# Kernel optimization log

Measured on AMD Instinct MI355X. Metric: run time of the kernel, lower is better.

Reference implementation:

```python
import jax, jax.numpy as jnp
import numpy as np

N = 100000   # nodes
E = 1600000  # edges (before self loops)
IN, HID, OUT = 128, 128, 64


def setup_inputs() -> dict:
    key = jax.random.key(0)
    ks = jax.random.split(key, 5)
    x = jax.random.normal(ks[0], (N, IN), dtype=jnp.float32)
    edge_index = jax.random.randint(ks[1], (2, E), 0, N, dtype=jnp.int32)
    W1 = jax.random.normal(ks[2], (IN, HID), dtype=jnp.float32) * (1.0 / np.sqrt(IN))
    b1 = jnp.zeros((HID,), dtype=jnp.float32)
    W2 = jax.random.normal(ks[3], (HID, OUT), dtype=jnp.float32) * (1.0 / np.sqrt(HID))
    b2 = jnp.zeros((OUT,), dtype=jnp.float32)
    return {"x": x, "edge_index": edge_index, "W1": W1, "b1": b1, "W2": W2, "b2": b2}


def _gcn_conv(x, W, b, src, dst, norm):
    # linear transform first (small GEMM), then normalized scatter-add aggregation
    h = x @ W                                   # [N, d_out]
    msg = h[src] * norm[:, None]                # [E+N, d_out] gathered messages
    agg = jax.ops.segment_sum(msg, dst, num_segments=N)
    return agg + b


def reference(x, edge_index, W1, b1, W2, b2):
    loops = jnp.arange(N, dtype=edge_index.dtype)
    src = jnp.concatenate([edge_index[0], loops])   # add self loops (PyG GCNConv default)
    dst = jnp.concatenate([edge_index[1], loops])
    # symmetric normalization D^{-1/2} (A+I) D^{-1/2}
    deg = jax.ops.segment_sum(jnp.ones_like(dst, dtype=x.dtype), dst, num_segments=N)
    dinv = jnp.where(deg > 0, jax.lax.rsqrt(deg), 0.0)
    norm = dinv[src] * dinv[dst]                # [E+N]

    h = _gcn_conv(x, W1, b1, src, dst, norm)
    h = jax.nn.relu(h)
    out = _gcn_conv(h, W2, b2, src, dst, norm)
    return out
```

## Files before the change

### kernel.cpp

```cpp
#include <hip/hip_runtime.h>
#include <hip/hip_bf16.h>

#define IN_DIM  128
#define HID_DIM 128
#define OUT_DIM 64

typedef unsigned short ushort_t;
struct ushort4_t { ushort_t x, y, z, w; };
typedef __attribute__((ext_vector_type(8))) short bf16x8;
typedef __attribute__((ext_vector_type(4))) float f32x4;

__device__ __forceinline__ float bf2f(ushort_t u) {
    return __uint_as_float(((unsigned int)u) << 16);
}
__device__ __forceinline__ short f2bf_s(float v) {
    __hip_bfloat16 t = __float2bfloat16(v);
    return *(short*)&t;
}
__device__ __forceinline__ unsigned int pack2(float a, float b) {
    return ((unsigned int)(ushort_t)f2bf_s(b) << 16) | (ushort_t)f2bf_s(a);
}

__global__ __launch_bounds__(256, 2) void fused_gemm1_count(
        const float* __restrict__ x, const float* __restrict__ W,
        unsigned int* __restrict__ h,
        const int* __restrict__ dst, int* __restrict__ cnt, int* __restrict__ rank,
        int N, int E, int NT) {
    const int bid = blockIdx.x;
    const int tid = threadIdx.x;

    if (bid & 1) {
        const int lane = tid & 63;
        const int m    = lane & 15;
        const int quad = lane >> 4;
        const int gw   = (bid >> 1) * 4 + (tid >> 6);
        const int NW   = 1024;

        bf16x8 a[8][4];
        #pragma unroll
        for (int ct = 0; ct < 8; ++ct)
            #pragma unroll
            for (int kc = 0; kc < 4; ++kc)
                #pragma unroll
                for (int j = 0; j < 8; ++j)
                    a[ct][kc][j] = f2bf_s(W[(size_t)(kc * 32 + quad * 8 + j) * HID_DIM + ct * 16 + m]);

        for (int t = gw; t < NT; t += NW) {
            const int n0 = t * 16;
            int node = n0 + m; if (node >= N) node = N - 1;
            const float* xr = x + (size_t)node * IN_DIM + quad * 8;
            f32x4 acc[8];
            #pragma unroll
            for (int ct = 0; ct < 8; ++ct) acc[ct] = (f32x4){0.f, 0.f, 0.f, 0.f};
            #pragma unroll
            for (int kc = 0; kc < 4; ++kc) {
                const float4 v0 = *(const float4*)(xr + kc * 32);
                const float4 v1 = *(const float4*)(xr + kc * 32 + 4);
                bf16x8 b;
                b[0] = f2bf_s(v0.x); b[1] = f2bf_s(v0.y); b[2] = f2bf_s(v0.z); b[3] = f2bf_s(v0.w);
                b[4] = f2bf_s(v1.x); b[5] = f2bf_s(v1.y); b[6] = f2bf_s(v1.z); b[7] = f2bf_s(v1.w);
                #pragma unroll
                for (int ct = 0; ct < 8; ++ct)
                    acc[ct] = __builtin_amdgcn_mfma_f32_16x16x32_bf16(a[ct][kc], b, acc[ct], 0, 0, 0);
            }
            if (n0 + m < N) {
                unsigned int* o = h + (size_t)(n0 + m) * (HID_DIM / 2) + quad * 2;
                #pragma unroll
                for (int ct = 0; ct < 8; ++ct) {
                    uint2 pv;
                    pv.x = pack2(acc[ct][0], acc[ct][1]);
                    pv.y = pack2(acc[ct][2], acc[ct][3]);
                    *(uint2*)(o + ct * 8) = pv;
                }
            }
        }
    } else {
        const int ct = (bid >> 1) * 256 + tid;
        const int CT = 256 * 256;
        const int nq = E >> 2;
        const int4* d4 = (const int4*)dst;
        for (int q = ct; q < nq; q += CT) {
            const int4 d = d4[q];
            int4 r;
            r.x = atomicAdd(&cnt[d.x], 1);
            r.y = atomicAdd(&cnt[d.y], 1);
            r.z = atomicAdd(&cnt[d.z], 1);
            r.w = atomicAdd(&cnt[d.w], 1);
            ((int4*)rank)[q] = r;
        }
        for (int e = (nq << 2) + ct; e < E; e += CT)
            rank[e] = atomicAdd(&cnt[dst[e]], 1);
    }
}

__global__ void scan_partial(const int* __restrict__ cnt, int* __restrict__ bsum,
                             float* __restrict__ dinv, int N) {
    __shared__ int wsum[4];
    const int t = threadIdx.x;
    const int base = blockIdx.x * 2048 + t * 8;
    int s = 0;
    #pragma unroll
    for (int i = 0; i < 8; ++i) {
        if (base + i < N) {
            const int c = cnt[base + i];
            dinv[base + i] = rsqrtf((float)(c + 1));
            s += (c + 3) & ~3;
        }
    }
    #pragma unroll
    for (int off = 32; off > 0; off >>= 1) s += __shfl_down(s, off);
    const int lane = t & 63, w = t >> 6;
    if (lane == 0) wsum[w] = s;
    __syncthreads();
    if (t == 0) bsum[blockIdx.x] = wsum[0] + wsum[1] + wsum[2] + wsum[3];
}

__global__ void scan_write(const int* __restrict__ cnt, const int* __restrict__ bsum,
                           int* __restrict__ row_start, int2* __restrict__ pack, int N) {
    __shared__ int wsum[4];
    __shared__ int blockoff;
    const int t = threadIdx.x;
    if (t < 64) {
        int a = 0;
        for (int idx = t; idx < blockIdx.x; idx += 64) a += bsum[idx];
        #pragma unroll
        for (int off = 32; off > 0; off >>= 1) a += __shfl_down(a, off);
        if (t == 0) blockoff = a;
    }
    const int base = blockIdx.x * 2048 + t * 8;
    int c[8], v[8];
    #pragma unroll
    for (int i = 0; i < 8; ++i) {
        c[i] = (base + i < N) ? cnt[base + i] : 0;
        v[i] = (c[i] + 3) & ~3;
    }
    int s = v[0] + v[1] + v[2] + v[3] + v[4] + v[5] + v[6] + v[7];
    const int lane = t & 63, w = t >> 6;
    int incl = s;
    #pragma unroll
    for (int off = 1; off < 64; off <<= 1) {
        int u = __shfl_up(incl, off);
        if (lane >= off) incl += u;
    }
    if (lane == 63) wsum[w] = incl;
    __syncthreads();
    int woff = 0;
    for (int i = 0; i < w; ++i) woff += wsum[i];
    int run = blockoff + woff + (incl - s);
    const int2 zr = {0, 0};
    #pragma unroll
    for (int i = 0; i < 8; ++i) {
        if (base + i < N) {
            row_start[base + i] = run;
            for (int p = c[i]; p < v[i]; ++p) pack[run + p] = zr;
            run += v[i];
        }
    }
}

__global__ void fill_pack4(const int* __restrict__ src, const int* __restrict__ dst,
                           const int* __restrict__ rank, const int* __restrict__ row_start,
                           const float* __restrict__ dinv, int E, int2* __restrict__ pack) {
    const int q = blockIdx.x * blockDim.x + threadIdx.x;
    const int nq = E >> 2;
    if (q < nq) {
        const int4 s = ((const int4*)src)[q];
        const int4 d = ((const int4*)dst)[q];
        const int4 r = ((const int4*)rank)[q];
        int2 p;
        p.x = s.x; p.y = __float_as_int(dinv[s.x] * dinv[d.x]);
        pack[row_start[d.x] + r.x] = p;
        p.x = s.y; p.y = __float_as_int(dinv[s.y] * dinv[d.y]);
        pack[row_start[d.y] + r.y] = p;
        p.x = s.z; p.y = __float_as_int(dinv[s.z] * dinv[d.z]);
        pack[row_start[d.z] + r.z] = p;
        p.x = s.w; p.y = __float_as_int(dinv[s.w] * dinv[d.w]);
        pack[row_start[d.w] + r.w] = p;
    }
    if (q == 0) {
        for (int e = nq << 2; e < E; ++e) {
            int2 p;
            p.x = src[e]; p.y = __float_as_int(dinv[src[e]] * dinv[dst[e]]);
            pack[row_start[dst[e]] + rank[e]] = p;
        }
    }
}

__global__ __launch_bounds__(256) void gemm2_mfma(
        const ushort_t* __restrict__ agg,
        const float* __restrict__ W2, unsigned int* __restrict__ h2,
        int N, int NT, int NW) {
    const int tid  = threadIdx.x;
    const int lane = tid & 63;
    const int m    = lane & 15;
    const int quad = lane >> 4;
    const int gw   = blockIdx.x * 4 + (tid >> 6);

    bf16x8 a[4][4];
    #pragma unroll
    for (int ct = 0; ct < 4; ++ct)
        #pragma unroll
        for (int kc = 0; kc < 4; ++kc)
            #pragma unroll
            for (int j = 0; j < 8; ++j)
                a[ct][kc][j] = f2bf_s(W2[(size_t)(kc * 32 + quad * 8 + j) * OUT_DIM + ct * 16 + m]);

    for (int t = gw; t < NT; t += NW) {
        const int n0 = t * 16;
        int node = n0 + m; if (node >= N) node = N - 1;
        const ushort_t* ar = agg + (size_t)node * HID_DIM + quad * 8;
        f32x4 acc[4];
        #pragma unroll
        for (int ct = 0; ct < 4; ++ct) acc[ct] = (f32x4){0.f, 0.f, 0.f, 0.f};
        #pragma unroll
        for (int kc = 0; kc < 4; ++kc) {
            const bf16x8 b = *(const bf16x8*)(ar + kc * 32);
            #pragma unroll
            for (int ct = 0; ct < 4; ++ct)
                acc[ct] = __builtin_amdgcn_mfma_f32_16x16x32_bf16(a[ct][kc], b, acc[ct], 0, 0, 0);
        }
        if (n0 + m < N) {
            unsigned int* o = h2 + (size_t)(n0 + m) * (OUT_DIM / 2) + quad * 2;
            #pragma unroll
            for (int ct = 0; ct < 4; ++ct) {
                uint2 pv;
                pv.x = pack2(acc[ct][0], acc[ct][1]);
                pv.y = pack2(acc[ct][2], acc[ct][3]);
                *(uint2*)(o + ct * 8) = pv;
            }
        }
    }
}

template<int D, bool BF16_OUT, bool RELU>
__global__ void gather_bf16(const ushort_t* __restrict__ h, const int2* __restrict__ pack,
                            const int* __restrict__ row_start, const int* __restrict__ cnt,
                            const float* __restrict__ dinv, const float* __restrict__ bias,
                            int N, void* __restrict__ outv) {
    const int TPN = D / 4;
    const int NPB = 256 / TPN;
    const int t = threadIdx.x;
    const int node = blockIdx.x * NPB + t / TPN;
    if (node >= N) return;
    const int f = (t & (TPN - 1)) * 4;
    const float dd = dinv[node];

    const ushort4_t self = *(const ushort4_t*)(h + (size_t)node * D + f);
    const float sn = dd * dd;
    float4 acc;
    acc.x = bf2f(self.x) * sn; acc.y = bf2f(self.y) * sn;
    acc.z = bf2f(self.z) * sn; acc.w = bf2f(self.w) * sn;
    const float4 bv = *(const float4*)(bias + f);
    acc.x += bv.x; acc.y += bv.y; acc.z += bv.z; acc.w += bv.w;

    const int2* pk = pack + row_start[node];
    const int cpad = (cnt[node] + 3) & ~3;
    for (int e = 0; e < cpad; e += 4) {
        const int4 a = *(const int4*)(pk + e);
        const int4 b = *(const int4*)(pk + e + 2);
        {
            const ushort4_t v = *(const ushort4_t*)(h + (size_t)a.x * D + f);
            const float n = __int_as_float(a.y);
            acc.x += bf2f(v.x) * n; acc.y += bf2f(v.y) * n;
            acc.z += bf2f(v.z) * n; acc.w += bf2f(v.w) * n;
        }
        {
            const ushort4_t v = *(const ushort4_t*)(h + (size_t)a.z * D + f);
            const float n = __int_as_float(a.w);
            acc.x += bf2f(v.x) * n; acc.y += bf2f(v.y) * n;
            acc.z += bf2f(v.z) * n; acc.w += bf2f(v.w) * n;
        }
        {
            const ushort4_t v = *(const ushort4_t*)(h + (size_t)b.x * D + f);
            const float n = __int_as_float(b.y);
            acc.x += bf2f(v.x) * n; acc.y += bf2f(v.y) * n;
            acc.z += bf2f(v.z) * n; acc.w += bf2f(v.w) * n;
        }
        {
            const ushort4_t v = *(const ushort4_t*)(h + (size_t)b.z * D + f);
            const float n = __int_as_float(b.w);
            acc.x += bf2f(v.x) * n; acc.y += bf2f(v.y) * n;
            acc.z += bf2f(v.z) * n; acc.w += bf2f(v.w) * n;
        }
    }
    if (RELU) {
        acc.x = fmaxf(acc.x, 0.f); acc.y = fmaxf(acc.y, 0.f);
        acc.z = fmaxf(acc.z, 0.f); acc.w = fmaxf(acc.w, 0.f);
    }
    if (BF16_OUT) {
        unsigned int* out = (unsigned int*)outv;
        uint2 pv;
        pv.x = pack2(acc.x, acc.y);
        pv.y = pack2(acc.z, acc.w);
        *(uint2*)(out + ((size_t)node * D + f) / 2) = pv;
    } else {
        float* out = (float*)outv;
        *(float4*)(out + (size_t)node * D + f) = acc;
    }
}

extern "C" void kernel_launch(void* const* d_in, const int* in_sizes, int n_in,
                              void* d_out, int out_size, void* d_ws, size_t ws_size,
                              hipStream_t stream) {
    const float* x   = (const float*)d_in[0];
    const int*   ei  = (const int*)  d_in[1];
    const float* W1  = (const float*)d_in[2];
    const float* b1  = (const float*)d_in[3];
    const float* W2  = (const float*)d_in[4];
    const float* b2  = (const float*)d_in[5];
    float* out = (float*)d_out;

    const int N = in_sizes[0] / IN_DIM;
    const int E = in_sizes[1] / 2;
    const int* src = ei;
    const int* dst = ei + E;

    const int PACK_CAP = E + 4 * N;
    float* dinv      = (float*)d_ws;
    int*   cnt       = (int*)(dinv + N);
    int*   row_start = cnt + N;
    int*   bsum      = row_start + N;
    size_t off       = (size_t)(3 * N + 1024);
    off = (off + 3) & ~(size_t)3;
    int2*  pack      = (int2*)((int*)d_ws + off);
    unsigned int* h1 = (unsigned int*)(pack + PACK_CAP);
    unsigned int* agg1 = h1 + (size_t)N * (HID_DIM / 2);
    int*   rank      = (int*)agg1;
    unsigned int* h2 = h1;

    const int B = 256;
    const int S = (N + 2047) / 2048;
    const int NT = (N + 15) / 16;

    hipMemsetAsync(cnt, 0, (size_t)N * sizeof(int), stream);
    fused_gemm1_count<<<512, 256, 0, stream>>>(x, W1, h1, dst, cnt, rank, N, E, NT);

    scan_partial<<<S, 256, 0, stream>>>(cnt, bsum, dinv, N);
    scan_write<<<S, 256, 0, stream>>>(cnt, bsum, row_start, pack, N);

    fill_pack4<<<((E >> 2) + B - 1) / B, B, 0, stream>>>(src, dst, rank, row_start, dinv, E, pack);

    gather_bf16<HID_DIM, true, true><<<(N + 7) / 8, 256, 0, stream>>>(
        (const ushort_t*)h1, pack, row_start, cnt, dinv, b1, N, (void*)agg1);

    gemm2_mfma<<<768, 256, 0, stream>>>(
        (const ushort_t*)agg1, W2, h2, N, NT, 768 * 4);

    gather_bf16<OUT_DIM, false, false><<<(N + 15) / 16, 256, 0, stream>>>(
        (const ushort_t*)h2, pack, row_start, cnt, dinv, b2, N, (void*)out);
}
```

Baseline: 312.2 us.

## Replace atomic CSR build with two-level bucket sort by destination

```diff
diff --git a/kernel.cpp b/kernel.cpp
--- a/kernel.cpp
+++ b/kernel.cpp
@@ -4,6 +4,8 @@
 #define IN_DIM  128
 #define HID_DIM 128
 #define OUT_DIM 64
+#define NBUK 1024
+#define NB1  256
 
 typedef unsigned short ushort_t;
 struct ushort4_t { ushort_t x, y, z, w; };
@@ -21,121 +23,160 @@
     return ((unsigned int)(ushort_t)f2bf_s(b) << 16) | (ushort_t)f2bf_s(a);
 }
 
-__global__ __launch_bounds__(256, 2) void fused_gemm1_count(
+__global__ __launch_bounds__(256, 2) void gemm1_mfma(
         const float* __restrict__ x, const float* __restrict__ W,
-        unsigned int* __restrict__ h,
-        const int* __restrict__ dst, int* __restrict__ cnt, int* __restrict__ rank,
-        int N, int E, int NT) {
-    const int bid = blockIdx.x;
-    const int tid = threadIdx.x;
-
-    if (bid & 1) {
-        const int lane = tid & 63;
-        const int m    = lane & 15;
-        const int quad = lane >> 4;
-        const int gw   = (bid >> 1) * 4 + (tid >> 6);
-        const int NW   = 1024;
-
-        bf16x8 a[8][4];
-        #pragma unroll
-        for (int ct = 0; ct < 8; ++ct)
-            #pragma unroll
-            for (int kc = 0; kc < 4; ++kc)
-                #pragma unroll
-                for (int j = 0; j < 8; ++j)
-                    a[ct][kc][j] = f2bf_s(W[(size_t)(kc * 32 + quad * 8 + j) * HID_DIM + ct * 16 + m]);
-
-        for (int t = gw; t < NT; t += NW) {
-            const int n0 = t * 16;
-            int node = n0 + m; if (node >= N) node = N - 1;
-            const float* xr = x + (size_t)node * IN_DIM + quad * 8;
-            f32x4 acc[8];
-            #pragma unroll
-            for (int ct = 0; ct < 8; ++ct) acc[ct] = (f32x4){0.f, 0.f, 0.f, 0.f};
-            #pragma unroll
-            for (int kc = 0; kc < 4; ++kc) {
-                const float4 v0 = *(const float4*)(xr + kc * 32);
-                const float4 v1 = *(const float4*)(xr + kc * 32 + 4);
-                bf16x8 b;
-                b[0] = f2bf_s(v0.x); b[1] = f2bf_s(v0.y); b[2] = f2bf_s(v0.z); b[3] = f2bf_s(v0.w);
-                b[4] = f2bf_s(v1.x); b[5] = f2bf_s(v1.y); b[6] = f2bf_s(v1.z); b[7] = f2bf_s(v1.w);
-                #pragma unroll
-                for (int ct = 0; ct < 8; ++ct)
-                    acc[ct] = __builtin_amdgcn_mfma_f32_16x16x32_bf16(a[ct][kc], b, acc[ct], 0, 0, 0);
+        unsigned int* __restrict__ h, int N, int NT, int NW) {
+    const int tid  = threadIdx.x;
+    const int lane = tid & 63;
+    const int m    = lane & 15;
+    const int quad = lane >> 4;
+    const int gw   = blockIdx.x * 4 + (tid >> 6);
+
+    bf16x8 a[8][4];
+    #pragma unroll
+    for (int ct = 0; ct < 8; ++ct)
+        #pragma unroll
+        for (int kc = 0; kc < 4; ++kc)
+            #pragma unroll
+            for (int j = 0; j < 8; ++j)
+                a[ct][kc][j] = f2bf_s(W[(size_t)(kc * 32 + quad * 8 + j) * HID_DIM + ct * 16 + m]);
+
+    for (int t = gw; t < NT; t += NW) {
+        const int n0 = t * 16;
+        int node = n0 + m; if (node >= N) node = N - 1;
+        const float* xr = x + (size_t)node * IN_DIM + quad * 8;
+        f32x4 acc[8];
+        #pragma unroll
+        for (int ct = 0; ct < 8; ++ct) acc[ct] = (f32x4){0.f, 0.f, 0.f, 0.f};
+        #pragma unroll
+        for (int kc = 0; kc < 4; ++kc) {
+            const float4 v0 = *(const float4*)(xr + kc * 32);
+            const float4 v1 = *(const float4*)(xr + kc * 32 + 4);
+            bf16x8 b;
+            b[0] = f2bf_s(v0.x); b[1] = f2bf_s(v0.y); b[2] = f2bf_s(v0.z); b[3] = f2bf_s(v0.w);
+            b[4] = f2bf_s(v1.x); b[5] = f2bf_s(v1.y); b[6] = f2bf_s(v1.z); b[7] = f2bf_s(v1.w);
+            #pragma unroll
+            for (int ct = 0; ct < 8; ++ct)
+                acc[ct] = __builtin_amdgcn_mfma_f32_16x16x32_bf16(a[ct][kc], b, acc[ct], 0, 0, 0);
+        }
+        if (n0 + m < N) {
+            unsigned int* o = h + (size_t)(n0 + m) * (HID_DIM / 2) + quad * 2;
+            #pragma unroll
+            for (int ct = 0; ct < 8; ++ct) {
+                uint2 pv;
+                pv.x = pack2(acc[ct][0], acc[ct][1]);
+                pv.y = pack2(acc[ct][2], acc[ct][3]);
+                *(uint2*)(o + ct * 8) = pv;
             }
-            if (n0 + m < N) {
-                unsigned int* o = h + (size_t)(n0 + m) * (HID_DIM / 2) + quad * 2;
-                #pragma unroll
-                for (int ct = 0; ct < 8; ++ct) {
-                    uint2 pv;
-                    pv.x = pack2(acc[ct][0], acc[ct][1]);
-                    pv.y = pack2(acc[ct][2], acc[ct][3]);
-                    *(uint2*)(o + ct * 8) = pv;
-                }
-            }
-        }
-    } else {
-        const int ct = (bid >> 1) * 256 + tid;
-        const int CT = 256 * 256;
-        const int nq = E >> 2;
-        const int4* d4 = (const int4*)dst;
-        for (int q = ct; q < nq; q += CT) {
-            const int4 d = d4[q];
-            int4 r;
-            r.x = atomicAdd(&cnt[d.x], 1);
-            r.y = atomicAdd(&cnt[d.y], 1);
-            r.z = atomicAdd(&cnt[d.z], 1);
-            r.w = atomicAdd(&cnt[d.w], 1);
-            ((int4*)rank)[q] = r;
-        }
-        for (int e = (nq << 2) + ct; e < E; e += CT)
-            rank[e] = atomicAdd(&cnt[dst[e]], 1);
-    }
-}
-
-__global__ void scan_partial(const int* __restrict__ cnt, int* __restrict__ bsum,
-                             float* __restrict__ dinv, int N) {
+        }
+    }
+}
+
+__global__ void bucket_hist(const int* __restrict__ dst, int E, int CH, int* __restrict__ mat) {
+    __shared__ int hist[NBUK];
+    const int t = threadIdx.x;
+    for (int i = t; i < NBUK; i += 256) hist[i] = 0;
+    __syncthreads();
+    const int lo = blockIdx.x * CH;
+    const int hi = min(lo + CH, E);
+    for (int e = lo + t; e < hi; e += 256)
+        atomicAdd(&hist[dst[e] >> 7], 1);
+    __syncthreads();
+    for (int i = t; i < NBUK; i += 256) mat[blockIdx.x * NBUK + i] = hist[i];
+}
+
+__global__ void mat_scan(int* __restrict__ mat, int* __restrict__ bbase, int* __restrict__ bcnt) {
+    __shared__ int lsum[NBUK];
+    __shared__ int wsum[16];
+    const int t = threadIdx.x;
+    int run = 0;
+    for (int b = 0; b < NB1; ++b) {
+        const int idx = b * NBUK + t;
+        const int v = mat[idx];
+        mat[idx] = run;
+        run += v;
+    }
+    lsum[t] = run;
+    __syncthreads();
+    const int lane = t & 63, w = t >> 6;
+    int incl = lsum[t];
+    #pragma unroll
+    for (int off = 1; off < 64; off <<= 1) {
+        int u = __shfl_up(incl, off);
+        if (lane >= off) incl += u;
+    }
+    if (lane == 63) wsum[w] = incl;
+    __syncthreads();
+    int woff = 0;
+    for (int i = 0; i < w; ++i) woff += wsum[i];
+    const int excl = woff + incl - lsum[t];
+    bbase[t] = excl;
+    bcnt[t]  = lsum[t];
+    if (t == NBUK - 1) bbase[NBUK] = excl + lsum[t];
+    __syncthreads();
+    for (int b = 0; b < NB1; ++b) mat[b * NBUK + t] += excl;
+}
+
+__global__ void bucket_scatter(const int* __restrict__ src, const int* __restrict__ dst,
+                               int E, int CH, const int* __restrict__ mat, int2* __restrict__ ebuf) {
+    __shared__ int lofs[NBUK];
+    const int t = threadIdx.x;
+    for (int i = t; i < NBUK; i += 256) lofs[i] = mat[blockIdx.x * NBUK + i];
+    __syncthreads();
+    const int lo = blockIdx.x * CH;
+    const int hi = min(lo + CH, E);
+    for (int e = lo + t; e < hi; e += 256) {
+        const int d = dst[e];
+        const int pos = atomicAdd(&lofs[d >> 7], 1);
+        int2 sd; sd.x = src[e]; sd.y = d;
+        ebuf[pos] = sd;
+    }
+}
+
+__global__ void bucket_count(const int2* __restrict__ ebuf, const int* __restrict__ bbase,
+                             const int* __restrict__ bcnt, int* __restrict__ cnt, int N) {
+    __shared__ int lcnt[128];
+    const int t = threadIdx.x;
+    if (t < 128) lcnt[t] = 0;
+    __syncthreads();
+    const int b = blockIdx.x;
+    const int base = bbase[b], n = bcnt[b];
+    for (int e = t; e < n; e += 256)
+        atomicAdd(&lcnt[ebuf[base + e].y & 127], 1);
+    __syncthreads();
+    const int node0 = b << 7;
+    if (t < 128 && node0 + t < N) cnt[node0 + t] = lcnt[t];
+}
+
+__global__ void scan_fused(const int* __restrict__ cnt, float* __restrict__ dinv,
+                           int* __restrict__ row_start, int N) {
     __shared__ int wsum[4];
-    const int t = threadIdx.x;
-    const int base = blockIdx.x * 2048 + t * 8;
-    int s = 0;
-    #pragma unroll
-    for (int i = 0; i < 8; ++i) {
-        if (base + i < N) {
-            const int c = cnt[base + i];
-            dinv[base + i] = rsqrtf((float)(c + 1));
-            s += (c + 3) & ~3;
-        }
-    }
-    #pragma unroll
-    for (int off = 32; off > 0; off >>= 1) s += __shfl_down(s, off);
+    __shared__ int sh_off;
+    const int t = threadIdx.x;
+    const int base0 = blockIdx.x * 2048;
+
+    int pre = 0;
+    for (int i = t * 4; i < base0; i += 1024) {
+        const int4 c4 = *(const int4*)(cnt + i);
+        pre += ((c4.x + 3) & ~3) + ((c4.y + 3) & ~3) + ((c4.z + 3) & ~3) + ((c4.w + 3) & ~3);
+    }
+    #pragma unroll
+    for (int off = 32; off > 0; off >>= 1) pre += __shfl_down(pre, off);
     const int lane = t & 63, w = t >> 6;
-    if (lane == 0) wsum[w] = s;
-    __syncthreads();
-    if (t == 0) bsum[blockIdx.x] = wsum[0] + wsum[1] + wsum[2] + wsum[3];
-}
-
-__global__ void scan_write(const int* __restrict__ cnt, const int* __restrict__ bsum,
-                           int* __restrict__ row_start, int2* __restrict__ pack, int N) {
-    __shared__ int wsum[4];
-    __shared__ int blockoff;
-    const int t = threadIdx.x;
-    if (t < 64) {
-        int a = 0;
-        for (int idx = t; idx < blockIdx.x; idx += 64) a += bsum[idx];
-        #pragma unroll
-        for (int off = 32; off > 0; off >>= 1) a += __shfl_down(a, off);
-        if (t == 0) blockoff = a;
-    }
-    const int base = blockIdx.x * 2048 + t * 8;
+    if (lane == 0) wsum[w] = pre;
+    __syncthreads();
+    if (t == 0) sh_off = wsum[0] + wsum[1] + wsum[2] + wsum[3];
+    __syncthreads();
+
+    const int base = base0 + t * 8;
     int c[8], v[8];
     #pragma unroll
     for (int i = 0; i < 8; ++i) {
         c[i] = (base + i < N) ? cnt[base + i] : 0;
         v[i] = (c[i] + 3) & ~3;
+        if (base + i < N) dinv[base + i] = rsqrtf((float)(c[i] + 1));
     }
     int s = v[0] + v[1] + v[2] + v[3] + v[4] + v[5] + v[6] + v[7];
-    const int lane = t & 63, w = t >> 6;
     int incl = s;
     #pragma unroll
     for (int off = 1; off < 64; off <<= 1) {
@@ -146,42 +187,81 @@
     __syncthreads();
     int woff = 0;
     for (int i = 0; i < w; ++i) woff += wsum[i];
-    int run = blockoff + woff + (incl - s);
-    const int2 zr = {0, 0};
+    int run = sh_off + woff + (incl - s);
     #pragma unroll
     for (int i = 0; i < 8; ++i) {
         if (base + i < N) {
             row_start[base + i] = run;
-            for (int p = c[i]; p < v[i]; ++p) pack[run + p] = zr;
             run += v[i];
         }
     }
 }
 
-__global__ void fill_pack4(const int* __restrict__ src, const int* __restrict__ dst,
-                           const int* __restrict__ rank, const int* __restrict__ row_start,
-                           const float* __restrict__ dinv, int E, int2* __restrict__ pack) {
-    const int q = blockIdx.x * blockDim.x + threadIdx.x;
-    const int nq = E >> 2;
-    if (q < nq) {
-        const int4 s = ((const int4*)src)[q];
-        const int4 d = ((const int4*)dst)[q];
-        const int4 r = ((const int4*)rank)[q];
-        int2 p;
-        p.x = s.x; p.y = __float_as_int(dinv[s.x] * dinv[d.x]);
-        pack[row_start[d.x] + r.x] = p;
-        p.x = s.y; p.y = __float_as_int(dinv[s.y] * dinv[d.y]);
-        pack[row_start[d.y] + r.y] = p;
-        p.x = s.z; p.y = __float_as_int(dinv[s.z] * dinv[d.z]);
-        pack[row_start[d.z] + r.z] = p;
-        p.x = s.w; p.y = __float_as_int(dinv[s.w] * dinv[d.w]);
-        pack[row_start[d.w] + r.w] = p;
-    }
-    if (q == 0) {
-        for (int e = nq << 2; e < E; ++e) {
-            int2 p;
-            p.x = src[e]; p.y = __float_as_int(dinv[src[e]] * dinv[dst[e]]);
-            pack[row_start[dst[e]] + rank[e]] = p;
+#define REGCAP 3072
+__global__ void bucket_build(const int2* __restrict__ ebuf, const int* __restrict__ bbase,
+                             const int* __restrict__ bcnt, const int* __restrict__ row_start,
+                             const int* __restrict__ cnt, const float* __restrict__ dinv,
+                             int N, int2* __restrict__ pack) {
+    __shared__ __align__(16) int2 reg[REGCAP];
+    __shared__ int lofs[128];
+    __shared__ int lrank[128];
+    __shared__ float dv[128];
+    __shared__ int s_regLen;
+    const int t = threadIdx.x;
+    const int b = blockIdx.x;
+    const int node0 = b << 7;
+    const int nn = min(128, N - node0);
+    if (t < nn) {
+        lofs[t]  = row_start[node0 + t];
+        lrank[t] = 0;
+        dv[t]    = dinv[node0 + t];
+    }
+    __syncthreads();
+    const int base = lofs[0];
+    if (t == 0) {
+        const int lastc = cnt[node0 + nn - 1];
+        s_regLen = (lofs[nn - 1] - base) + ((lastc + 3) & ~3);
+    }
+    __syncthreads();
+    const int regLen = s_regLen;
+    if (t < nn) lofs[t] -= base;
+    __syncthreads();
+
+    const int ebase = bbase[b], en = bcnt[b];
+    if (regLen <= REGCAP) {
+        for (int e = t; e < en; e += 256) {
+            const int2 sd = ebuf[ebase + e];
+            const int i = sd.y & 127;
+            const int r = atomicAdd(&lrank[i], 1);
+            int2 p; p.x = sd.x;
+            p.y = __float_as_int(dinv[sd.x] * dv[i]);
+            reg[lofs[i] + r] = p;
+        }
+        __syncthreads();
+        for (int i = t; i < nn; i += 256) {
+            const int c = lrank[i];
+            const int v = (c + 3) & ~3;
+            for (int p = c; p < v; ++p) reg[lofs[i] + p] = (int2){0, 0};
+        }
+        __syncthreads();
+        const int n4 = regLen >> 1;
+        const int4* s4 = (const int4*)reg;
+        int4* d4 = (int4*)(pack + base);
+        for (int k = t; k < n4; k += 256) d4[k] = s4[k];
+    } else {
+        for (int e = t; e < en; e += 256) {
+            const int2 sd = ebuf[ebase + e];
+            const int i = sd.y & 127;
+            const int r = atomicAdd(&lrank[i], 1);
+            int2 p; p.x = sd.x;
+            p.y = __float_as_int(dinv[sd.x] * dv[i]);
+            pack[base + lofs[i] + r] = p;
+        }
+        __syncthreads();
+        for (int i = t; i < nn; i += 256) {
+            const int c = lrank[i];
+            const int v = (c + 3) & ~3;
+            for (int p = c; p < v; ++p) pack[base + lofs[i] + p] = (int2){0, 0};
         }
     }
 }
@@ -319,26 +399,32 @@
     float* dinv      = (float*)d_ws;
     int*   cnt       = (int*)(dinv + N);
     int*   row_start = cnt + N;
-    int*   bsum      = row_start + N;
-    size_t off       = (size_t)(3 * N + 1024);
+    int*   bbase     = row_start + N;
+    int*   bcnt      = bbase + (NBUK + 1);
+    int*   mat       = bcnt + NBUK;
+    size_t off       = (size_t)(3 * N) + (NBUK + 1) + NBUK + (size_t)NB1 * NBUK;
     off = (off + 3) & ~(size_t)3;
     int2*  pack      = (int2*)((int*)d_ws + off);
     unsigned int* h1 = (unsigned int*)(pack + PACK_CAP);
     unsigned int* agg1 = h1 + (size_t)N * (HID_DIM / 2);
-    int*   rank      = (int*)agg1;
+    int2*  ebuf      = (int2*)agg1;
     unsigned int* h2 = h1;
 
-    const int B = 256;
-    const int S = (N + 2047) / 2048;
-    const int NT = (N + 15) / 16;
-
-    hipMemsetAsync(cnt, 0, (size_t)N * sizeof(int), stream);
-    fused_gemm1_count<<<512, 256, 0, stream>>>(x, W1, h1, dst, cnt, rank, N, E, NT);
-
-    scan_partial<<<S, 256, 0, stream>>>(cnt, bsum, dinv, N);
-    scan_write<<<S, 256, 0, stream>>>(cnt, bsum, row_start, pack, N);
-
-    fill_pack4<<<((E >> 2) + B - 1) / B, B, 0, stream>>>(src, dst, rank, row_start, dinv, E, pack);
+    const int S   = (N + 2047) / 2048;
+    const int NT  = (N + 15) / 16;
+    const int NBK = (N + 127) >> 7;
+    const int CH  = (E + NB1 - 1) / NB1;
+
+    gemm1_mfma<<<1568, 256, 0, stream>>>(x, W1, h1, N, NT, 1568 * 4);
+
+    bucket_hist<<<NB1, 256, 0, stream>>>(dst, E, CH, mat);
+    mat_scan<<<1, 1024, 0, stream>>>(mat, bbase, bcnt);
+    bucket_scatter<<<NB1, 256, 0, stream>>>(src, dst, E, CH, mat, ebuf);
+    bucket_count<<<NBK, 256, 0, stream>>>(ebuf, bbase, bcnt, cnt, N);
+
+    scan_fused<<<S, 256, 0, stream>>>(cnt, dinv, row_start, N);
+
+    bucket_build<<<NBK, 256, 0, stream>>>(ebuf, bbase, bcnt, row_start, cnt, dinv, N, pack);
 
     gather_bf16<HID_DIM, true, true><<<(N + 7) / 8, 256, 0, stream>>>(
         (const ushort_t*)h1, pack, row_start, cnt, dinv, b1, N, (void*)agg1);
```

After: 412.1 us. +32.0%, slower.

## Fuse layer-1 gather with GEMM2 via LDS tile; merge scan kernels

Applied to the files above, without the earlier changes.

```diff
diff --git a/kernel.cpp b/kernel.cpp
--- a/kernel.cpp
+++ b/kernel.cpp
@@ -7,6 +7,7 @@
 
 typedef unsigned short ushort_t;
 struct ushort4_t { ushort_t x, y, z, w; };
+struct __align__(16) ushort8_t { ushort_t u[8]; };
 typedef __attribute__((ext_vector_type(8))) short bf16x8;
 typedef __attribute__((ext_vector_type(4))) float f32x4;
 
@@ -93,49 +94,35 @@
     }
 }
 
-__global__ void scan_partial(const int* __restrict__ cnt, int* __restrict__ bsum,
-                             float* __restrict__ dinv, int N) {
-    __shared__ int wsum[4];
-    const int t = threadIdx.x;
-    const int base = blockIdx.x * 2048 + t * 8;
-    int s = 0;
-    #pragma unroll
-    for (int i = 0; i < 8; ++i) {
-        if (base + i < N) {
-            const int c = cnt[base + i];
-            dinv[base + i] = rsqrtf((float)(c + 1));
-            s += (c + 3) & ~3;
-        }
-    }
-    #pragma unroll
-    for (int off = 32; off > 0; off >>= 1) s += __shfl_down(s, off);
-    const int lane = t & 63, w = t >> 6;
-    if (lane == 0) wsum[w] = s;
-    __syncthreads();
-    if (t == 0) bsum[blockIdx.x] = wsum[0] + wsum[1] + wsum[2] + wsum[3];
-}
-
-__global__ void scan_write(const int* __restrict__ cnt, const int* __restrict__ bsum,
+__global__ void scan_fused(const int* __restrict__ cnt, float* __restrict__ dinv,
                            int* __restrict__ row_start, int2* __restrict__ pack, int N) {
     __shared__ int wsum[4];
-    __shared__ int blockoff;
+    __shared__ int sh_off;
     const int t = threadIdx.x;
-    if (t < 64) {
-        int a = 0;
-        for (int idx = t; idx < blockIdx.x; idx += 64) a += bsum[idx];
-        #pragma unroll
-        for (int off = 32; off > 0; off >>= 1) a += __shfl_down(a, off);
-        if (t == 0) blockoff = a;
-    }
-    const int base = blockIdx.x * 2048 + t * 8;
+    const int base0 = blockIdx.x * 2048;
+
+    int pre = 0;
+    for (int i = t * 4; i < base0; i += 1024) {
+        const int4 c4 = *(const int4*)(cnt + i);
+        pre += ((c4.x + 3) & ~3) + ((c4.y + 3) & ~3) + ((c4.z + 3) & ~3) + ((c4.w + 3) & ~3);
+    }
+    #pragma unroll
+    for (int off = 32; off > 0; off >>= 1) pre += __shfl_down(pre, off);
+    const int lane = t & 63, w = t >> 6;
+    if (lane == 0) wsum[w] = pre;
+    __syncthreads();
+    if (t == 0) sh_off = wsum[0] + wsum[1] + wsum[2] + wsum[3];
+    __syncthreads();
+
+    const int base = base0 + t * 8;
     int c[8], v[8];
     #pragma unroll
     for (int i = 0; i < 8; ++i) {
         c[i] = (base + i < N) ? cnt[base + i] : 0;
         v[i] = (c[i] + 3) & ~3;
+        if (base + i < N) dinv[base + i] = rsqrtf((float)(c[i] + 1));
     }
     int s = v[0] + v[1] + v[2] + v[3] + v[4] + v[5] + v[6] + v[7];
-    const int lane = t & 63, w = t >> 6;
     int incl = s;
     #pragma unroll
     for (int off = 1; off < 64; off <<= 1) {
@@ -146,7 +133,7 @@
     __syncthreads();
     int woff = 0;
     for (int i = 0; i < w; ++i) woff += wsum[i];
-    int run = blockoff + woff + (incl - s);
+    int run = sh_off + woff + (incl - s);
     const int2 zr = {0, 0};
     #pragma unroll
     for (int i = 0; i < 8; ++i) {
@@ -186,49 +173,90 @@
     }
 }
 
-__global__ __launch_bounds__(256) void gemm2_mfma(
-        const ushort_t* __restrict__ agg,
+__global__ __launch_bounds__(256) void gather128_gemm2(
+        const ushort_t* __restrict__ h, const int2* __restrict__ pack,
+        const int* __restrict__ row_start, const int* __restrict__ cnt,
+        const float* __restrict__ dinv, const float* __restrict__ b1,
         const float* __restrict__ W2, unsigned int* __restrict__ h2,
-        int N, int NT, int NW) {
+        int N, int NT2, int NBLK) {
+    __shared__ ushort_t tile[16][136];
     const int tid  = threadIdx.x;
     const int lane = tid & 63;
+    const int wid  = tid >> 6;
     const int m    = lane & 15;
     const int quad = lane >> 4;
-    const int gw   = blockIdx.x * 4 + (tid >> 6);
-
-    bf16x8 a[4][4];
-    #pragma unroll
-    for (int ct = 0; ct < 4; ++ct)
+
+    bf16x8 a[4];
+    #pragma unroll
+    for (int kc = 0; kc < 4; ++kc)
         #pragma unroll
-        for (int kc = 0; kc < 4; ++kc)
+        for (int j = 0; j < 8; ++j)
+            a[kc][j] = f2bf_s(W2[(size_t)(kc * 32 + quad * 8 + j) * OUT_DIM + wid * 16 + m]);
+
+    const int gn = tid >> 4;
+    const int f0 = (tid & 15) * 8;
+
+    for (int t = blockIdx.x; t < NT2; t += NBLK) {
+        const int n0 = t * 16;
+        int node = n0 + gn; if (node >= N) node = N - 1;
+        const float dd = dinv[node];
+        float accv[8];
+        {
+            const float sn = dd * dd;
+            const ushort8_t hv = *(const ushort8_t*)(h + (size_t)node * HID_DIM + f0);
             #pragma unroll
-            for (int j = 0; j < 8; ++j)
-                a[ct][kc][j] = f2bf_s(W2[(size_t)(kc * 32 + quad * 8 + j) * OUT_DIM + ct * 16 + m]);
-
-    for (int t = gw; t < NT; t += NW) {
-        const int n0 = t * 16;
-        int node = n0 + m; if (node >= N) node = N - 1;
-        const ushort_t* ar = agg + (size_t)node * HID_DIM + quad * 8;
-        f32x4 acc[4];
+            for (int i = 0; i < 8; ++i) accv[i] = bf2f(hv.u[i]) * sn + b1[f0 + i];
+        }
+        const int2* pk = pack + row_start[node];
+        const int cpad = (cnt[node] + 3) & ~3;
+        for (int e = 0; e < cpad; e += 4) {
+            const int4 pa = *(const int4*)(pk + e);
+            const int4 pb = *(const int4*)(pk + e + 2);
+            {
+                const ushort8_t v = *(const ushort8_t*)(h + (size_t)pa.x * HID_DIM + f0);
+                const float n = __int_as_float(pa.y);
+                #pragma unroll
+                for (int i = 0; i < 8; ++i) accv[i] += bf2f(v.u[i]) * n;
+            }
+            {
+                const ushort8_t v = *(const ushort8_t*)(h + (size_t)pa.z * HID_DIM + f0);
+                const float n = __int_as_float(pa.w);
+                #pragma unroll
+                for (int i = 0; i < 8; ++i) accv[i] += bf2f(v.u[i]) * n;
+            }
+            {
+                const ushort8_t v = *(const ushort8_t*)(h + (size_t)pb.x * HID_DIM + f0);
+                const float n = __int_as_float(pb.y);
+                #pragma unroll
+                for (int i = 0; i < 8; ++i) accv[i] += bf2f(v.u[i]) * n;
+            }
+            {
+                const ushort8_t v = *(const ushort8_t*)(h + (size_t)pb.z * HID_DIM + f0);
+                const float n = __int_as_float(pb.w);
+                #pragma unroll
+                for (int i = 0; i < 8; ++i) accv[i] += bf2f(v.u[i]) * n;
+            }
+        }
+        ushort8_t pv;
         #pragma unroll
-        for (int ct = 0; ct < 4; ++ct) acc[ct] = (f32x4){0.f, 0.f, 0.f, 0.f};
+        for (int i = 0; i < 8; ++i) pv.u[i] = (ushort_t)f2bf_s(fmaxf(accv[i], 0.f));
+        *(ushort8_t*)&tile[gn][f0] = pv;
+        __syncthreads();
+
+        f32x4 acc = (f32x4){0.f, 0.f, 0.f, 0.f};
         #pragma unroll
         for (int kc = 0; kc < 4; ++kc) {
-            const bf16x8 b = *(const bf16x8*)(ar + kc * 32);
-            #pragma unroll
-            for (int ct = 0; ct < 4; ++ct)
-                acc[ct] = __builtin_amdgcn_mfma_f32_16x16x32_bf16(a[ct][kc], b, acc[ct], 0, 0, 0);
+            const bf16x8 b = *(const bf16x8*)&tile[m][kc * 32 + quad * 8];
+            acc = __builtin_amdgcn_mfma_f32_16x16x32_bf16(a[kc], b, acc, 0, 0, 0);
         }
         if (n0 + m < N) {
-            unsigned int* o = h2 + (size_t)(n0 + m) * (OUT_DIM / 2) + quad * 2;
-            #pragma unroll
-            for (int ct = 0; ct < 4; ++ct) {
-                uint2 pv;
-                pv.x = pack2(acc[ct][0], acc[ct][1]);
-                pv.y = pack2(acc[ct][2], acc[ct][3]);
-                *(uint2*)(o + ct * 8) = pv;
-            }
-        }
+            unsigned int* o = h2 + (size_t)(n0 + m) * (OUT_DIM / 2) + wid * 8 + quad * 2;
+            uint2 ov;
+            ov.x = pack2(acc[0], acc[1]);
+            ov.y = pack2(acc[2], acc[3]);
+            *(uint2*)o = ov;
+        }
+        __syncthreads();
     }
 }
 
@@ -319,14 +347,13 @@
     float* dinv      = (float*)d_ws;
     int*   cnt       = (int*)(dinv + N);
     int*   row_start = cnt + N;
-    int*   bsum      = row_start + N;
-    size_t off       = (size_t)(3 * N + 1024);
+    size_t off       = (size_t)(3 * N);
     off = (off + 3) & ~(size_t)3;
     int2*  pack      = (int2*)((int*)d_ws + off);
     unsigned int* h1 = (unsigned int*)(pack + PACK_CAP);
-    unsigned int* agg1 = h1 + (size_t)N * (HID_DIM / 2);
-    int*   rank      = (int*)agg1;
+    int*   rank      = (int*)(h1 + (size_t)N * (HID_DIM / 2));
     unsigned int* h2 = h1;
+    unsigned int* h2_safe = (unsigned int*)(rank + E);
 
     const int B = 256;
     const int S = (N + 2047) / 2048;
@@ -335,17 +362,13 @@
     hipMemsetAsync(cnt, 0, (size_t)N * sizeof(int), stream);
     fused_gemm1_count<<<512, 256, 0, stream>>>(x, W1, h1, dst, cnt, rank, N, E, NT);
 
-    scan_partial<<<S, 256, 0, stream>>>(cnt, bsum, dinv, N);
-    scan_write<<<S, 256, 0, stream>>>(cnt, bsum, row_start, pack, N);
+    scan_fused<<<S, 256, 0, stream>>>(cnt, dinv, row_start, pack, N);
 
     fill_pack4<<<((E >> 2) + B - 1) / B, B, 0, stream>>>(src, dst, rank, row_start, dinv, E, pack);
 
-    gather_bf16<HID_DIM, true, true><<<(N + 7) / 8, 256, 0, stream>>>(
-        (const ushort_t*)h1, pack, row_start, cnt, dinv, b1, N, (void*)agg1);
-
-    gemm2_mfma<<<768, 256, 0, stream>>>(
-        (const ushort_t*)agg1, W2, h2, N, NT, 768 * 4);
+    gather128_gemm2<<<1024, 256, 0, stream>>>(
+        (const ushort_t*)h1, pack, row_start, cnt, dinv, b1, W2, h2_safe, N, NT, 1024);
 
     gather_bf16<OUT_DIM, false, false><<<(N + 15) / 16, 256, 0, stream>>>(
-        (const ushort_t*)h2, pack, row_start, cnt, dinv, b2, N, (void*)out);
-}
+        (const ushort_t*)h2_safe, pack, row_start, cnt, dinv, b2, N, (void*)out);
+}
```

Result: no change. 313.4 us (+0.4%).
